# Optimization experiments

Measured on AMD Instinct MI355X. Metric: run time of the kernel, lower is better.

The kernel has to match this reference:

```python
import jax, jax.numpy as jnp
import numpy as np


def _conv1x1(x, w, b):
    # x: [B,C,D,H,W], w: [O,C], b: [O] -> [B,O,D,H,W]
    return jnp.einsum('bcdhw,oc->bodhw', x, w) + b[None, :, None, None, None]


def setup_inputs() -> dict:
    key = jax.random.key(0)
    ks = jax.random.split(key, 8)
    C, Cr = 64, 8  # in_channels, in_channels // 8
    B, D, H, W = 2, 8, 32, 32
    s = 0.05
    return {
        'x': jax.random.normal(ks[0], (B, C, D, H, W), jnp.float32),
        'w_b': jax.random.normal(ks[1], (Cr, C), jnp.float32) * s,
        'b_b': jnp.zeros((Cr,), jnp.float32),
        'w_c': jax.random.normal(ks[2], (Cr, C), jnp.float32) * s,
        'b_c': jnp.zeros((Cr,), jnp.float32),
        'w_d': jax.random.normal(ks[3], (C, C), jnp.float32) * s,
        'b_d': jnp.zeros((C,), jnp.float32),
        'alpha': jnp.zeros((1,), jnp.float32),
    }


def reference(x, w_b, b_b, w_c, b_c, w_d, b_d, alpha):
    B, C, D, H, W = x.shape
    N = D * H * W
    feat_b = _conv1x1(x, w_b, b_b).reshape(B, -1, N).transpose(0, 2, 1)  # [B,N,Cr]
    feat_c = _conv1x1(x, w_c, b_c).reshape(B, -1, N)                      # [B,Cr,N]
    attn = jax.nn.softmax(jnp.einsum('bnk,bkm->bnm', feat_b, feat_c), axis=-1)  # [B,N,N]
    feat_d = _conv1x1(x, w_d, b_d).reshape(B, -1, N)                      # [B,C,N]
    # feat_d @ attn^T  -> [B,C,N]
    feat_e = jnp.einsum('bcn,bmn->bcm', feat_d, attn).reshape(B, C, D, H, W)
    return alpha[0] * feat_e + x
```

## Files before the change

### kernel.cpp

```cpp
#include <hip/hip_runtime.h>


#define NB   2
#define CH   64
#define CR   8
#define NPOS 8192
#define QB   64
#define KB2  512
#define NSTR (NPOS / KB2)

typedef __attribute__((ext_vector_type(8)))  __bf16 bf16x8;
typedef __attribute__((ext_vector_type(16))) float  f32x16;

__device__ inline unsigned pk_bf(float lo, float hi) {
    unsigned r;
    asm("v_cvt_pk_bf16_f32 %0, %1, %2" : "=v"(r) : "v"(lo), "v"(hi));
    return r;
}
__device__ inline unsigned short f2bf(float v) {
    return (unsigned short)(pk_bf(v, 0.f) & 0xFFFFu);
}
union U4B { uint4 u; bf16x8 b; };
__device__ inline bf16x8 as_bf(uint4 u) { U4B x; x.u = u; return x.b; }

__global__ __launch_bounds__(128) void proj_kernel(
    const float* __restrict__ x,
    const float* __restrict__ w_b, const float* __restrict__ b_b,
    const float* __restrict__ w_c,
    const float* __restrict__ w_d,
    unsigned short* __restrict__ Qb, unsigned short* __restrict__ Kb,
    unsigned short* __restrict__ VTb)
{
    __shared__ unsigned short wt[96 * 64];
    const int tid = threadIdx.x;
    const float L2E = 1.4426950408889634f;
    for (int j = tid; j < 4096; j += 128) wt[j] = f2bf(w_d[j]);
    for (int j = tid; j < 512; j += 128) {
        wt[64 * 64 + j] = f2bf(w_b[j] * L2E);
        wt[72 * 64 + j] = f2bf(w_c[j]);
    }
    __syncthreads();

    const int w  = tid >> 6, l = tid & 63, li = l & 31, h = l >> 5;
    const int ng = blockIdx.x * 64 + w * 32;
    const int b  = ng >> 13;
    const int n  = ng & (NPOS - 1);

    const f32x16 z16 = {0,0,0,0,0,0,0,0,0,0,0,0,0,0,0,0};

    uint4 af[3][4];
    #pragma unroll
    for (int t = 0; t < 3; ++t)
        #pragma unroll
        for (int ks = 0; ks < 4; ++ks)
            af[t][ks] = *(const uint4*)&wt[(t * 32 + li) * 64 + ks * 16 + 8 * h];

    f32x16 acc0 = z16, acc1 = z16, acc2 = z16;
    #pragma unroll
    for (int ks = 0; ks < 4; ++ks) {
        float xr[8];
        #pragma unroll
        for (int j = 0; j < 8; ++j)
            xr[j] = x[(size_t)(b * CH + ks * 16 + 8 * h + j) * NPOS + n + li];
        uint4 bf = make_uint4(pk_bf(xr[0], xr[1]), pk_bf(xr[2], xr[3]),
                              pk_bf(xr[4], xr[5]), pk_bf(xr[6], xr[7]));
        acc0 = __builtin_amdgcn_mfma_f32_32x32x16_bf16(as_bf(af[0][ks]), as_bf(bf), acc0, 0, 0, 0);
        acc1 = __builtin_amdgcn_mfma_f32_32x32x16_bf16(as_bf(af[1][ks]), as_bf(bf), acc1, 0, 0, 0);
        acc2 = __builtin_amdgcn_mfma_f32_32x32x16_bf16(as_bf(af[2][ks]), as_bf(bf), acc2, 0, 0, 0);
    }

    #pragma unroll
    for (int r = 0; r < 16; ++r) {
        int crow = (r & 3) + 8 * (r >> 2) + 4 * h;
        VTb[(size_t)(b * CH + crow) * NPOS + n + li]      = f2bf(acc0[r]);
        VTb[(size_t)(b * CH + 32 + crow) * NPOS + n + li] = f2bf(acc1[r]);
    }

    {
        float bb0 = b_b[4 * h + 0] * L2E, bb1 = b_b[4 * h + 1] * L2E;
        float bb2 = b_b[4 * h + 2] * L2E, bb3 = b_b[4 * h + 3] * L2E;
        unsigned q0p = pk_bf(acc2[0] + bb0, acc2[1] + bb1);
        unsigned q1p = pk_bf(acc2[2] + bb2, acc2[3] + bb3);
        unsigned k0p = pk_bf(acc2[4], acc2[5]);
        unsigned k1p = pk_bf(acc2[6], acc2[7]);
        unsigned qa0 = q0p, qb0 = q0p, qa1 = q1p, qb1 = q1p;
        asm("v_permlane32_swap_b32 %0, %1" : "+v"(qa0), "+v"(qb0));
        asm("v_permlane32_swap_b32 %0, %1" : "+v"(qa1), "+v"(qb1));
        unsigned ka0 = k0p, kb0 = k0p, ka1 = k1p, kb1 = k1p;
        asm("v_permlane32_swap_b32 %0, %1" : "+v"(ka0), "+v"(kb0));
        asm("v_permlane32_swap_b32 %0, %1" : "+v"(ka1), "+v"(kb1));
        if (h == 0) {
            *(uint4*)(Qb + (size_t)(b * NPOS + n + li) * CR) = make_uint4(qa0, qa1, qb0, qb1);
            *(uint4*)(Kb + (size_t)(b * NPOS + n + li) * CR) = make_uint4(ka0, ka1, kb0, kb1);
        }
    }
}

__global__ __launch_bounds__(1024, 4) void attn_kernel(
    const unsigned short* __restrict__ Qb, const unsigned short* __restrict__ Kb,
    const unsigned short* __restrict__ VTb, const float* __restrict__ x,
    const float* __restrict__ alpha, const float* __restrict__ b_d,
    float* __restrict__ out)
{
    __shared__ uint4 sbuf[8192];
    float* mbuf = (float*)sbuf;

    const int tid = threadIdx.x;
    const int w   = tid >> 6;
    const int l   = tid & 63;
    const int li  = l & 31;
    const int h   = l >> 5;
    const int qh  = w & 1;
    const int kh  = w >> 1;
    const int blk = (blockIdx.x & 7) * 32 + (blockIdx.x >> 3);
    const int b   = blk >> 7;
    const int q0  = (blk & 127) * QB;
    const int m   = q0 + 32 * qh + li;

    const f32x16 z16 = {0,0,0,0,0,0,0,0,0,0,0,0,0,0,0,0};
    const uint4 zero4 = make_uint4(0, 0, 0, 0);

    uint4 qf = zero4;
    if (h == 0) qf = *(const uint4*)(Qb + ((size_t)b * NPOS + m) * CR);

    f32x16 acc0 = z16, acc1 = z16;
    float dn0 = 0.f, dn1 = 0.f, dn2 = 0.f, dn3 = 0.f;

    const unsigned short* kb0 = Kb + ((size_t)b * NPOS + kh * 64 + li) * CR;
    const unsigned short* kb1 = kb0 + 32 * CR;

    const unsigned short* vg = VTb + ((size_t)(b * CH + w)) * NPOS
                             + (size_t)((l & 56) | ((l & 7) ^ (w & 7))) * 8;

#define STAGE(T) {                                                               \
    const unsigned short* g_ = vg + (size_t)(T) * KB2;                           \
    const int bb_ = ((T) & 1) * 65536 + w * 1024;                                \
    _Pragma("unroll")                                                            \
    for (int r_ = 0; r_ < 4; ++r_)                                               \
        __builtin_amdgcn_global_load_lds(                                        \
            (const __attribute__((address_space(1))) void*)(g_ + (size_t)r_ * 16 * NPOS), \
            (__attribute__((address_space(3))) void*)((char*)(void*)sbuf + bb_ + r_ * 16384), \
            16, 0, 0); }

    const int i0 = li * 64 + ((kh * 8 + h) ^ (li & 7));

#define CHUNK(IA, KF) {                                                                       \
    f32x16 sv = __builtin_amdgcn_mfma_f32_32x32x16_bf16(as_bf(KF), as_bf(qf), z16, 0, 0, 0);  \
    const int bs_ = (t & 1) * 4096;                                                           \
    uint4 a00 = sbuf[bs_ + (IA)];                                                             \
    uint4 a01 = sbuf[bs_ + ((IA) ^ 2)];                                                       \
    uint4 a10 = sbuf[bs_ + 2048 + (IA)];                                                      \
    uint4 a11 = sbuf[bs_ + 2048 + ((IA) ^ 2)];                                                \
    float p_[16];                                                                             \
    _Pragma("unroll")                                                                         \
    for (int r_ = 0; r_ < 16; ++r_) p_[r_] = __builtin_amdgcn_exp2f(sv[r_]);                  \
    dn0 += (p_[0]  + p_[1])  + (p_[2]  + p_[3]);                                              \
    dn1 += (p_[4]  + p_[5])  + (p_[6]  + p_[7]);                                              \
    dn2 += (p_[8]  + p_[9])  + (p_[10] + p_[11]);                                             \
    dn3 += (p_[12] + p_[13]) + (p_[14] + p_[15]);                                             \
    unsigned pa0 = pk_bf(p_[0],  p_[1]),  pa1 = pk_bf(p_[2],  p_[3]);                         \
    unsigned pb0 = pk_bf(p_[4],  p_[5]),  pb1 = pk_bf(p_[6],  p_[7]);                         \
    unsigned pc0 = pk_bf(p_[8],  p_[9]),  pc1 = pk_bf(p_[10], p_[11]);                        \
    unsigned pd0 = pk_bf(p_[12], p_[13]), pd1 = pk_bf(p_[14], p_[15]);                        \
    asm("v_permlane32_swap_b32 %0, %1" : "+v"(pa0), "+v"(pb0));                               \
    asm("v_permlane32_swap_b32 %0, %1" : "+v"(pa1), "+v"(pb1));                               \
    asm("v_permlane32_swap_b32 %0, %1" : "+v"(pc0), "+v"(pd0));                               \
    asm("v_permlane32_swap_b32 %0, %1" : "+v"(pc1), "+v"(pd1));                               \
    uint4 BA = make_uint4(pa0, pa1, pb0, pb1);                                                \
    uint4 BB = make_uint4(pc0, pc1, pd0, pd1);                                                \
    acc0 = __builtin_amdgcn_mfma_f32_32x32x16_bf16(as_bf(a00), as_bf(BA), acc0, 0, 0, 0);     \
    acc0 = __builtin_amdgcn_mfma_f32_32x32x16_bf16(as_bf(a01), as_bf(BB), acc0, 0, 0, 0);     \
    acc1 = __builtin_amdgcn_mfma_f32_32x32x16_bf16(as_bf(a10), as_bf(BA), acc1, 0, 0, 0);     \
    acc1 = __builtin_amdgcn_mfma_f32_32x32x16_bf16(as_bf(a11), as_bf(BB), acc1, 0, 0, 0); }

    STAGE(0);
    uint4 kf0 = zero4, kf1 = zero4;
    if (h == 0) { kf0 = *(const uint4*)kb0; kf1 = *(const uint4*)kb1; }
    __syncthreads();

    for (int t = 0; t < NSTR; ++t) {
        uint4 kn0 = zero4, kn1 = zero4;
        if (t + 1 < NSTR) {
            STAGE(t + 1);
            if (h == 0) {
                size_t ko = (size_t)(t + 1) * KB2 * CR;
                kn0 = *(const uint4*)(kb0 + ko);
                kn1 = *(const uint4*)(kb1 + ko);
            }
        }
        CHUNK(i0, kf0);
        CHUNK(i0 ^ 4, kf1);
        __syncthreads();
        kf0 = kn0; kf1 = kn1;
    }
#undef STAGE
#undef CHUNK

    float den = (dn0 + dn1) + (dn2 + dn3);
    den += __shfl_xor(den, 32);

    for (int g = 0; g < 2; ++g) {
        for (int step = 4; step >= 1; step >>= 1) {
            if (qh == g && kh >= step && kh < 2 * step) {
                float* rg = mbuf + (kh - step) * 2080;
                #pragma unroll
                for (int r = 0; r < 16; ++r) {
                    rg[r * 64 + l]        = acc0[r];
                    rg[1024 + r * 64 + l] = acc1[r];
                }
                if (h == 0) rg[2048 + li] = den;
            }
            __syncthreads();
            if (qh == g && kh < step) {
                const float* rg = mbuf + kh * 2080;
                #pragma unroll
                for (int r = 0; r < 16; ++r) {
                    acc0[r] += rg[r * 64 + l];
                    acc1[r] += rg[1024 + r * 64 + l];
                }
                if (h == 0) den += rg[2048 + li];
            }
            __syncthreads();
        }
    }
    if (kh == 0) {
        float* rg = mbuf + qh * 2080;
        #pragma unroll
        for (int r = 0; r < 16; ++r) {
            rg[r * 64 + l]        = acc0[r];
            rg[1024 + r * 64 + l] = acc1[r];
        }
        if (h == 0) rg[2048 + li] = den;
    }
    __syncthreads();

    {
        const int c   = tid >> 4;
        const int q4  = (tid & 15) * 4;
        const int qhe = q4 >> 5, qlo = q4 & 31;
        const int tile = c >> 5, c5 = c & 31;
        const int hh  = (c5 >> 2) & 1;
        const int r   = (c5 & 3) | ((c5 >> 3) << 2);
        const float* rg = mbuf + qhe * 2080;
        float4 a   = *(const float4*)&rg[tile * 1024 + r * 64 + 32 * hh + qlo];
        float4 dnv = *(const float4*)&rg[2048 + qlo];
        float  al  = alpha[0];
        float  albd = al * b_d[c];
        size_t xo  = ((size_t)(b * CH + c)) * NPOS + q0 + q4;
        float4 xv  = *(const float4*)&x[xo];
        float4 o;
        o.x = a.x * (al / dnv.x) + albd + xv.x;
        o.y = a.y * (al / dnv.y) + albd + xv.y;
        o.z = a.z * (al / dnv.z) + albd + xv.z;
        o.w = a.w * (al / dnv.w) + albd + xv.w;
        *(float4*)&out[xo] = o;
    }
}

extern "C" void kernel_launch(void* const* d_in, const int* in_sizes, int n_in,
                              void* d_out, int out_size, void* d_ws, size_t ws_size,
                              hipStream_t stream) {
    const float* x     = (const float*)d_in[0];
    const float* w_b   = (const float*)d_in[1];
    const float* b_b   = (const float*)d_in[2];
    const float* w_c   = (const float*)d_in[3];
    const float* w_d   = (const float*)d_in[5];
    const float* b_d   = (const float*)d_in[6];
    const float* alpha = (const float*)d_in[7];
    float* out = (float*)d_out;

    unsigned short* Qw  = (unsigned short*)d_ws;
    unsigned short* Kw  = Qw + (size_t)NB * NPOS * CR;
    unsigned short* VTw = Kw + (size_t)NB * NPOS * CR;

    proj_kernel<<<256, 128, 0, stream>>>(x, w_b, b_b, w_c, w_d, Qw, Kw, VTw);
    attn_kernel<<<NB * NPOS / QB, 1024, 0, stream>>>(Qw, Kw, VTw, x, alpha, b_d, out);
}
```

Before: 47.53 us.

## Store V in MFMA fragment layout and load directly to registers, dropping LDS staging

The projection kernel now writes V in a pre-swizzled fragment layout matching the MFMA A-operand, so the attention kernel can load each operand with one 16-byte global load per lane instead of staging through LDS with global_load_lds and block-wide barriers. The key range is split across the 8 key-groups contiguously (1024 keys each) with a two-deep register double buffer, and the exp/pack sequence is interleaved to reduce live registers. This removes the per-tile __syncthreads and the LDS traffic, and shrinks shared memory to the reduction buffer. The cost is that every wave reads V straight from global/L2 with no reuse through LDS, and the scattered 2-byte stores in the projection kernel may be less coalesced.

```diff
diff --git a/kernel.cpp b/kernel.cpp
--- a/kernel.cpp
+++ b/kernel.cpp
@@ -6,8 +6,6 @@
 #define CR   8
 #define NPOS 8192
 #define QB   64
-#define KB2  512
-#define NSTR (NPOS / KB2)
 
 typedef __attribute__((ext_vector_type(8)))  __bf16 bf16x8;
 typedef __attribute__((ext_vector_type(16))) float  f32x16;
@@ -29,7 +27,7 @@
     const float* __restrict__ w_c,
     const float* __restrict__ w_d,
     unsigned short* __restrict__ Qb, unsigned short* __restrict__ Kb,
-    unsigned short* __restrict__ VTb)
+    unsigned short* __restrict__ VFb)
 {
     __shared__ unsigned short wt[96 * 64];
     const int tid = threadIdx.x;
@@ -69,11 +67,17 @@
         acc2 = __builtin_amdgcn_mfma_f32_32x32x16_bf16(as_bf(af[2][ks]), as_bf(bf), acc2, 0, 0, 0);
     }
 
-    #pragma unroll
-    for (int r = 0; r < 16; ++r) {
-        int crow = (r & 3) + 8 * (r >> 2) + 4 * h;
-        VTb[(size_t)(b * CH + crow) * NPOS + n + li]      = f2bf(acc0[r]);
-        VTb[(size_t)(b * CH + 32 + crow) * NPOS + n + li] = f2bf(acc1[r]);
+    {
+        const int kb = n >> 5;
+        const int ks = ((li >> 4) << 1) | ((li >> 3) & 1);
+        unsigned short* vf = VFb + (size_t)b * NPOS * CH
+                           + (size_t)kb * 2048 + ks * 512 + (li & 7);
+        #pragma unroll
+        for (int r = 0; r < 16; ++r) {
+            int crow = (r & 3) + 8 * (r >> 2) + 4 * h;
+            vf[crow * 8]        = f2bf(acc0[r]);
+            vf[(32 + crow) * 8] = f2bf(acc1[r]);
+        }
     }
 
     {
@@ -98,12 +102,11 @@
 
 __global__ __launch_bounds__(1024, 4) void attn_kernel(
     const unsigned short* __restrict__ Qb, const unsigned short* __restrict__ Kb,
-    const unsigned short* __restrict__ VTb, const float* __restrict__ x,
+    const unsigned short* __restrict__ VFb, const float* __restrict__ x,
     const float* __restrict__ alpha, const float* __restrict__ b_d,
     float* __restrict__ out)
 {
-    __shared__ uint4 sbuf[8192];
-    float* mbuf = (float*)sbuf;
+    __shared__ float mbuf[4 * 2080];
 
     const int tid = threadIdx.x;
     const int w   = tid >> 6;
@@ -126,75 +129,61 @@
     f32x16 acc0 = z16, acc1 = z16;
     float dn0 = 0.f, dn1 = 0.f, dn2 = 0.f, dn3 = 0.f;
 
-    const unsigned short* kb0 = Kb + ((size_t)b * NPOS + kh * 64 + li) * CR;
-    const unsigned short* kb1 = kb0 + 32 * CR;
-
-    const unsigned short* vg = VTb + ((size_t)(b * CH + w)) * NPOS
-                             + (size_t)((l & 56) | ((l & 7) ^ (w & 7))) * 8;
-
-#define STAGE(T) {                                                               \
-    const unsigned short* g_ = vg + (size_t)(T) * KB2;                           \
-    const int bb_ = ((T) & 1) * 65536 + w * 1024;                                \
-    _Pragma("unroll")                                                            \
-    for (int r_ = 0; r_ < 4; ++r_)                                               \
-        __builtin_amdgcn_global_load_lds(                                        \
-            (const __attribute__((address_space(1))) void*)(g_ + (size_t)r_ * 16 * NPOS), \
-            (__attribute__((address_space(3))) void*)((char*)(void*)sbuf + bb_ + r_ * 16384), \
-            16, 0, 0); }
-
-    const int i0 = li * 64 + ((kh * 8 + h) ^ (li & 7));
-
-#define CHUNK(IA, KF) {                                                                       \
+    const unsigned short* kbp = Kb + ((size_t)b * NPOS + kh * 1024 + li) * CR;
+    const unsigned short* vfb = VFb + (size_t)b * NPOS * CH
+                              + (size_t)kh * 32 * 2048 + h * 512 + li * 8;
+
+#define LOADS(CC, KF, A00, A01, A10, A11) {                        \
+    const unsigned short* vp_ = vfb + (size_t)(CC) * 2048;         \
+    A00 = *(const uint4*)(vp_);                                    \
+    A01 = *(const uint4*)(vp_ + 1024);                             \
+    A10 = *(const uint4*)(vp_ + 256);                              \
+    A11 = *(const uint4*)(vp_ + 1280);                             \
+    if (h == 0) KF = *(const uint4*)(kbp + (size_t)(CC) * 32 * CR); }
+
+#define COMPUTE(KF, A00, A01, A10, A11) {                                                     \
     f32x16 sv = __builtin_amdgcn_mfma_f32_32x32x16_bf16(as_bf(KF), as_bf(qf), z16, 0, 0, 0);  \
-    const int bs_ = (t & 1) * 4096;                                                           \
-    uint4 a00 = sbuf[bs_ + (IA)];                                                             \
-    uint4 a01 = sbuf[bs_ + ((IA) ^ 2)];                                                       \
-    uint4 a10 = sbuf[bs_ + 2048 + (IA)];                                                      \
-    uint4 a11 = sbuf[bs_ + 2048 + ((IA) ^ 2)];                                                \
-    float p_[16];                                                                             \
-    _Pragma("unroll")                                                                         \
-    for (int r_ = 0; r_ < 16; ++r_) p_[r_] = __builtin_amdgcn_exp2f(sv[r_]);                  \
-    dn0 += (p_[0]  + p_[1])  + (p_[2]  + p_[3]);                                              \
-    dn1 += (p_[4]  + p_[5])  + (p_[6]  + p_[7]);                                              \
-    dn2 += (p_[8]  + p_[9])  + (p_[10] + p_[11]);                                             \
-    dn3 += (p_[12] + p_[13]) + (p_[14] + p_[15]);                                             \
-    unsigned pa0 = pk_bf(p_[0],  p_[1]),  pa1 = pk_bf(p_[2],  p_[3]);                         \
-    unsigned pb0 = pk_bf(p_[4],  p_[5]),  pb1 = pk_bf(p_[6],  p_[7]);                         \
-    unsigned pc0 = pk_bf(p_[8],  p_[9]),  pc1 = pk_bf(p_[10], p_[11]);                        \
-    unsigned pd0 = pk_bf(p_[12], p_[13]), pd1 = pk_bf(p_[14], p_[15]);                        \
+    float p0_, p1_;                                                                           \
+    unsigned pa0, pa1, pb0, pb1, pc0, pc1, pd0, pd1;                                          \
+    p0_ = __builtin_amdgcn_exp2f(sv[0]);  p1_ = __builtin_amdgcn_exp2f(sv[1]);                \
+    dn0 += p0_ + p1_;  pa0 = pk_bf(p0_, p1_);                                                 \
+    p0_ = __builtin_amdgcn_exp2f(sv[2]);  p1_ = __builtin_amdgcn_exp2f(sv[3]);                \
+    dn1 += p0_ + p1_;  pa1 = pk_bf(p0_, p1_);                                                 \
+    p0_ = __builtin_amdgcn_exp2f(sv[4]);  p1_ = __builtin_amdgcn_exp2f(sv[5]);                \
+    dn2 += p0_ + p1_;  pb0 = pk_bf(p0_, p1_);                                                 \
+    p0_ = __builtin_amdgcn_exp2f(sv[6]);  p1_ = __builtin_amdgcn_exp2f(sv[7]);                \
+    dn3 += p0_ + p1_;  pb1 = pk_bf(p0_, p1_);                                                 \
+    p0_ = __builtin_amdgcn_exp2f(sv[8]);  p1_ = __builtin_amdgcn_exp2f(sv[9]);                \
+    dn0 += p0_ + p1_;  pc0 = pk_bf(p0_, p1_);                                                 \
+    p0_ = __builtin_amdgcn_exp2f(sv[10]); p1_ = __builtin_amdgcn_exp2f(sv[11]);               \
+    dn1 += p0_ + p1_;  pc1 = pk_bf(p0_, p1_);                                                 \
+    p0_ = __builtin_amdgcn_exp2f(sv[12]); p1_ = __builtin_amdgcn_exp2f(sv[13]);               \
+    dn2 += p0_ + p1_;  pd0 = pk_bf(p0_, p1_);                                                 \
+    p0_ = __builtin_amdgcn_exp2f(sv[14]); p1_ = __builtin_amdgcn_exp2f(sv[15]);               \
+    dn3 += p0_ + p1_;  pd1 = pk_bf(p0_, p1_);                                                 \
     asm("v_permlane32_swap_b32 %0, %1" : "+v"(pa0), "+v"(pb0));                               \
     asm("v_permlane32_swap_b32 %0, %1" : "+v"(pa1), "+v"(pb1));                               \
     asm("v_permlane32_swap_b32 %0, %1" : "+v"(pc0), "+v"(pd0));                               \
     asm("v_permlane32_swap_b32 %0, %1" : "+v"(pc1), "+v"(pd1));                               \
     uint4 BA = make_uint4(pa0, pa1, pb0, pb1);                                                \
     uint4 BB = make_uint4(pc0, pc1, pd0, pd1);                                                \
-    acc0 = __builtin_amdgcn_mfma_f32_32x32x16_bf16(as_bf(a00), as_bf(BA), acc0, 0, 0, 0);     \
-    acc0 = __builtin_amdgcn_mfma_f32_32x32x16_bf16(as_bf(a01), as_bf(BB), acc0, 0, 0, 0);     \
-    acc1 = __builtin_amdgcn_mfma_f32_32x32x16_bf16(as_bf(a10), as_bf(BA), acc1, 0, 0, 0);     \
-    acc1 = __builtin_amdgcn_mfma_f32_32x32x16_bf16(as_bf(a11), as_bf(BB), acc1, 0, 0, 0); }
-
-    STAGE(0);
-    uint4 kf0 = zero4, kf1 = zero4;
-    if (h == 0) { kf0 = *(const uint4*)kb0; kf1 = *(const uint4*)kb1; }
-    __syncthreads();
-
-    for (int t = 0; t < NSTR; ++t) {
-        uint4 kn0 = zero4, kn1 = zero4;
-        if (t + 1 < NSTR) {
-            STAGE(t + 1);
-            if (h == 0) {
-                size_t ko = (size_t)(t + 1) * KB2 * CR;
-                kn0 = *(const uint4*)(kb0 + ko);
-                kn1 = *(const uint4*)(kb1 + ko);
-            }
-        }
-        CHUNK(i0, kf0);
-        CHUNK(i0 ^ 4, kf1);
-        __syncthreads();
-        kf0 = kn0; kf1 = kn1;
-    }
-#undef STAGE
-#undef CHUNK
+    acc0 = __builtin_amdgcn_mfma_f32_32x32x16_bf16(as_bf(A00), as_bf(BA), acc0, 0, 0, 0);     \
+    acc0 = __builtin_amdgcn_mfma_f32_32x32x16_bf16(as_bf(A01), as_bf(BB), acc0, 0, 0, 0);     \
+    acc1 = __builtin_amdgcn_mfma_f32_32x32x16_bf16(as_bf(A10), as_bf(BA), acc1, 0, 0, 0);     \
+    acc1 = __builtin_amdgcn_mfma_f32_32x32x16_bf16(as_bf(A11), as_bf(BB), acc1, 0, 0, 0); }
+
+    uint4 kfA = zero4, a00A, a01A, a10A, a11A;
+    uint4 kfB = zero4, a00B, a01B, a10B, a11B;
+    LOADS(0, kfA, a00A, a01A, a10A, a11A);
+
+    for (int cc = 0; cc < 32; cc += 2) {
+        LOADS(cc + 1, kfB, a00B, a01B, a10B, a11B);
+        COMPUTE(kfA, a00A, a01A, a10A, a11A);
+        if (cc + 2 < 32) LOADS(cc + 2, kfA, a00A, a01A, a10A, a11A);
+        COMPUTE(kfB, a00B, a01B, a10B, a11B);
+    }
+#undef LOADS
+#undef COMPUTE
 
     float den = (dn0 + dn1) + (dn2 + dn3);
     den += __shfl_xor(den, 32);
@@ -271,8 +260,8 @@
 
     unsigned short* Qw  = (unsigned short*)d_ws;
     unsigned short* Kw  = Qw + (size_t)NB * NPOS * CR;
-    unsigned short* VTw = Kw + (size_t)NB * NPOS * CR;
-
-    proj_kernel<<<256, 128, 0, stream>>>(x, w_b, b_b, w_c, w_d, Qw, Kw, VTw);
-    attn_kernel<<<NB * NPOS / QB, 1024, 0, stream>>>(Qw, Kw, VTw, x, alpha, b_d, out);
-}
+    unsigned short* VFw = Kw + (size_t)NB * NPOS * CR;
+
+    proj_kernel<<<256, 128, 0, stream>>>(x, w_b, b_b, w_c, w_d, Qw, Kw, VFw);
+    attn_kernel<<<NB * NPOS / QB, 1024, 0, stream>>>(Qw, Kw, VFw, x, alpha, b_d, out);
+}
```

Measured after the change: 44.84 us. 1.06x faster.
